# Kernel optimization log

Hardware: AMD Instinct MI355X
Metric: run time of the kernel (lower is better)

Reference implementation:

```python
import jax, jax.numpy as jnp
import numpy as np

N, E, IN, HID, H, G = 50000, 400000, 128, 16, 11, 64
HC = HID * H  # 176
OUT, NC = 32, 10
EPS = 1e-5


def setup_inputs() -> dict:
    key = jax.random.key(0)
    ks = jax.random.split(key, 20)
    def n(i, shape, s=0.05):
        return jax.random.normal(ks[i], shape, jnp.float32) * s
    inp = {}
    inp["x"] = jax.random.normal(ks[0], (N, IN), jnp.float32)
    inp["edge_index"] = jax.random.randint(ks[1], (2, E), 0, N, dtype=jnp.int32)
    inp["batch"] = jnp.sort(jax.random.randint(ks[2], (N,), 0, G, dtype=jnp.int32))
    inp["W_pre"] = n(3, (IN, HC)); inp["b_pre"] = jnp.zeros((HC,), jnp.float32)
    # GraphNorm params for gn_pre, gn1..gn4 stacked: [5, HC]
    inp["gn_w"] = jnp.ones((5, HC), jnp.float32)
    inp["gn_b"] = jnp.zeros((5, HC), jnp.float32)
    inp["gn_ms"] = jnp.ones((5, HC), jnp.float32)  # mean_scale
    # conv1..conv4 (concat=True) stacked params
    inp["conv_Wl"] = n(4, (4, HC, HC)); inp["conv_Wr"] = n(5, (4, HC, HC))
    inp["conv_att"] = n(6, (4, H, HID))
    inp["conv_b"] = jnp.zeros((4, HC), jnp.float32)
    inp["conv_Wres"] = n(7, (4, HC, HC))
    # conv5 (concat=False -> out dim HID)
    inp["c5_Wl"] = n(8, (HC, HC)); inp["c5_Wr"] = n(9, (HC, HC))
    inp["c5_att"] = n(10, (H, HID))
    inp["c5_b"] = jnp.zeros((HID,), jnp.float32)
    inp["c5_Wres"] = n(11, (HC, HID))
    inp["W_o1"] = n(12, (HID, HID)); inp["b_o1"] = jnp.zeros((HID,), jnp.float32)
    inp["W_o2"] = n(13, (HID, OUT)); inp["b_o2"] = jnp.zeros((OUT,), jnp.float32)
    inp["W_cls"] = n(14, (OUT, NC)); inp["b_cls"] = jnp.zeros((NC,), jnp.float32)
    return inp


def graph_norm(x, w, b, ms, batch, cnt):
    # PyG GraphNorm: out = w * (x - ms*mean) / sqrt(var + eps) + b, stats per graph
    mean = jax.ops.segment_sum(x, batch, G) / cnt  # [G, F]
    xc = x - mean[batch] * ms
    var = jax.ops.segment_sum(xc * xc, batch, G) / cnt
    std = jnp.sqrt(var + EPS)
    return w * xc / std[batch] + b


def gatv2_conv(x, Wl, Wr, att, bias, Wres, src, dst, concat):
    # src/dst already include self-loops (PyG add_self_loops=True)
    xl = (x @ Wl).reshape(N, H, -1)  # source transform [N,H,C]
    xr = (x @ Wr).reshape(N, H, -1)  # target transform [N,H,C]
    e = jax.nn.leaky_relu(xl[src] + xr[dst], 0.2)          # [E',H,C]
    alpha = jnp.einsum('ehc,hc->eh', e, att)               # [E',H]
    amax = jax.ops.segment_max(alpha, dst, N)
    amax = jnp.where(jnp.isfinite(amax), amax, 0.0)
    ex = jnp.exp(alpha - amax[dst])
    den = jax.ops.segment_sum(ex, dst, N)
    a = ex / (den[dst] + 1e-16)
    out = jax.ops.segment_sum(xl[src] * a[..., None], dst, N)  # [N,H,C]
    out = out.reshape(N, -1) if concat else out.mean(axis=1)
    return out + x @ Wres + bias


def reference(x, edge_index, batch, W_pre, b_pre, gn_w, gn_b, gn_ms,
              conv_Wl, conv_Wr, conv_att, conv_b, conv_Wres,
              c5_Wl, c5_Wr, c5_att, c5_b, c5_Wres,
              W_o1, b_o1, W_o2, b_o2, W_cls, b_cls):
    loops = jnp.arange(N, dtype=edge_index.dtype)
    src = jnp.concatenate([edge_index[0], loops])
    dst = jnp.concatenate([edge_index[1], loops])
    cnt = jax.ops.segment_sum(jnp.ones((N, 1), jnp.float32), batch, G)
    cnt = jnp.maximum(cnt, 1.0)  # guard empty graphs

    h = x @ W_pre + b_pre
    h = graph_norm(h, gn_w[0], gn_b[0], gn_ms[0], batch, cnt)
    h = jax.nn.relu(h)
    for i in range(4):
        h = gatv2_conv(h, conv_Wl[i], conv_Wr[i], conv_att[i], conv_b[i],
                       conv_Wres[i], src, dst, concat=True)
        h = graph_norm(h, gn_w[i + 1], gn_b[i + 1], gn_ms[i + 1], batch, cnt)
        h = jax.nn.relu(h)
    h = gatv2_conv(h, c5_Wl, c5_Wr, c5_att, c5_b, c5_Wres, src, dst, concat=False)
    h = jax.nn.relu(h)
    h = jax.nn.relu(h @ W_o1 + b_o1)
    h = jax.nn.relu(h @ W_o2 + b_o2)
    return h @ W_cls + b_cls
```

## Files before the change

kernel.cpp:

```cpp
#include <hip/hip_runtime.h>
#include <math.h>

#define N_NODES 50000
#define N_EDGES 400000
#define IN_F 128
#define HC 176
#define NGRAPH 64
#define NBLK_ATTN 12500
#define NCHUNK 16

typedef _Float16 half8 __attribute__((ext_vector_type(8)));
typedef _Float16 half4 __attribute__((ext_vector_type(4)));
typedef float floatx4 __attribute__((ext_vector_type(4)));

__device__ inline float4 h4f(const _Float16* p) {
  half4 h = *(const half4*)p;
  return make_float4((float)h[0], (float)h[1], (float)h[2], (float)h[3]);
}

#define PREH 45056
#define MATH 67584
#define TOT_PAIRS 495616
#define KCBYTES 22528
#define GX8 49

__global__ void prep_kernel(const float* __restrict__ Wpre,
                            const float* __restrict__ cWl, const float* __restrict__ cWr,
                            const float* __restrict__ cWres,
                            const float* __restrict__ c5Wl, const float* __restrict__ c5Wr,
                            _Float16* __restrict__ wp) {
  int gid = blockIdx.x * 256 + threadIdx.x;
  if (gid >= TOT_PAIRS) return;
  int mat, idx;
  if (gid < 22528) { mat = 0; idx = gid; }
  else { int g = gid - 22528; mat = 1 + g / 33792; idx = g % 33792; }
  int kc = idx / 5632;
  int rem = idx - kc * 5632;
  int ct = rem / 512;
  int li = rem - ct * 512;
  int lane = li >> 3, j = li & 7;
  int k = kc * 32 + ((lane >> 4) << 3) + j;
  int col = ct * 16 + (lane & 15);
  const float* src; int Ksrc; size_t base;
  if (mat == 0) { src = Wpre; Ksrc = 128; base = 0; }
  else if (mat <= 12) {
    int lm = mat - 1; int layer = lm / 3; int sub = lm - layer * 3;
    const float* s = (sub == 0) ? cWl : (sub == 1) ? cWr : cWres;
    src = s + (size_t)layer * HC * HC; Ksrc = HC;
    base = PREH + (size_t)lm * MATH;
  } else {
    src = (mat == 13) ? c5Wl : c5Wr; Ksrc = HC;
    base = PREH + (size_t)12 * MATH + (size_t)(mat - 13) * MATH;
  }
  float v = (k < Ksrc) ? src[(size_t)k * HC + col] : 0.0f;
  _Float16 h = (_Float16)v;
  _Float16 l = (_Float16)(v - (float)h);
  size_t o = base + (size_t)(kc * 11 + ct) * 1024 + li;
  wp[o] = h;
  wp[o + 512] = l;
}

template <int MINW, bool DOSTATS, bool AHALF>
__global__ __launch_bounds__(256, MINW) void gemm_mfma_t(
    const float* __restrict__ A, int M, int K, int nkc, int nmat,
    const _Float16* __restrict__ Wp, int matStride,
    const float* __restrict__ scsh, const int* __restrict__ batch,
    const float* __restrict__ bias0, const float* __restrict__ bias1,
    const float* __restrict__ bias2,
    float* __restrict__ out0, float* __restrict__ out1, float* __restrict__ out2,
    float* __restrict__ parts, float* __restrict__ partq, float* __restrict__ stats,
    int halfMask) {
  __shared__ __align__(16) char smem[2 * KCBYTES];
  const int b = blockIdx.x;
  const int grp = b >> 3, sub = b & 7;
  const int mat = grp % nmat;
  const int tile = ((grp / nmat) << 3) | sub;
  if (tile * 128 >= M) return;
  const _Float16* W = Wp + (size_t)mat * matStride;
  float* outp = (mat == 0) ? out0 : (mat == 1) ? out1 : out2;
  const float* bias = (mat == 0) ? bias0 : (mat == 1) ? bias1 : bias2;
  const bool hOut = (halfMask >> mat) & 1;
  const int tid = threadIdx.x;
  const int lane = tid & 63;
  const int wv = tid >> 6;
  const int m16 = lane & 15, quad = lane >> 4;
  const int kb = quad << 3;
  const int rowBase = tile * 128 + wv * 32;
  const int rA0 = min(rowBase + m16, M - 1);
  const int rA1 = min(rowBase + 16 + m16, M - 1);
  const float* ap0 = A + (size_t)rA0 * K + kb;
  const float* ap1 = A + (size_t)rA1 * K + kb;
  const _Float16* hp0 = (const _Float16*)A + (size_t)rA0 * K + kb;
  const _Float16* hp1 = (const _Float16*)A + (size_t)rA1 * K + kb;
  const float* sc0 = nullptr; const float* sh0 = nullptr;
  const float* sc1 = nullptr; const float* sh1 = nullptr;
  if (scsh) {
    int g0 = batch[rA0], g1 = batch[rA1];
    sc0 = scsh + (size_t)g0 * HC + kb;
    sh0 = scsh + (size_t)(NGRAPH + g0) * HC + kb;
    sc1 = scsh + (size_t)g1 * HC + kb;
    sh1 = scsh + (size_t)(NGRAPH + g1) * HC + kb;
  }

  auto stage = [&](int kc, int buf) {
    const char* src = (const char*)W + (size_t)kc * KCBYTES;
    char* dst = smem + buf * KCBYTES;
#pragma unroll
    for (int i = 0; i < 6; i++) {
      int idx = wv * 6 + i;
      if (idx < 22) {
        __builtin_amdgcn_global_load_lds(
            (const __attribute__((address_space(1))) unsigned int*)(src + idx * 1024 + lane * 16),
            (__attribute__((address_space(3))) unsigned int*)(dst + idx * 1024),
            16, 0, 0);
      }
    }
  };

  floatx4 acc0[11], acc1[11];
#pragma unroll
  for (int ct = 0; ct < 11; ct++)
#pragma unroll
    for (int r = 0; r < 4; r++) { acc0[ct][r] = 0.0f; acc1[ct][r] = 0.0f; }

  stage(0, 0);

  for (int kc = 0; kc < nkc; kc++) {
    const int buf = kc & 1;
    __syncthreads();
    if (kc + 1 < nkc) stage(kc + 1, 1 - buf);

    const int koff = kc << 5;
    float va0[8], va1[8];
    if (koff + kb + 8 <= K) {
      if (AHALF) {
        half8 u = *(const half8*)(hp0 + koff);
        half8 w = *(const half8*)(hp1 + koff);
#pragma unroll
        for (int j = 0; j < 8; j++) { va0[j] = (float)u[j]; va1[j] = (float)w[j]; }
      } else {
        float4 u0 = *(const float4*)(ap0 + koff);
        float4 u1 = *(const float4*)(ap0 + koff + 4);
        float4 w0 = *(const float4*)(ap1 + koff);
        float4 w1 = *(const float4*)(ap1 + koff + 4);
        va0[0] = u0.x; va0[1] = u0.y; va0[2] = u0.z; va0[3] = u0.w;
        va0[4] = u1.x; va0[5] = u1.y; va0[6] = u1.z; va0[7] = u1.w;
        va1[0] = w0.x; va1[1] = w0.y; va1[2] = w0.z; va1[3] = w0.w;
        va1[4] = w1.x; va1[5] = w1.y; va1[6] = w1.z; va1[7] = w1.w;
      }
      if (scsh) {
        float s0[8], h0[8], s1[8], h1[8];
        float4 t;
        t = *(const float4*)(sc0 + koff);     s0[0]=t.x; s0[1]=t.y; s0[2]=t.z; s0[3]=t.w;
        t = *(const float4*)(sc0 + koff + 4); s0[4]=t.x; s0[5]=t.y; s0[6]=t.z; s0[7]=t.w;
        t = *(const float4*)(sh0 + koff);     h0[0]=t.x; h0[1]=t.y; h0[2]=t.z; h0[3]=t.w;
        t = *(const float4*)(sh0 + koff + 4); h0[4]=t.x; h0[5]=t.y; h0[6]=t.z; h0[7]=t.w;
        t = *(const float4*)(sc1 + koff);     s1[0]=t.x; s1[1]=t.y; s1[2]=t.z; s1[3]=t.w;
        t = *(const float4*)(sc1 + koff + 4); s1[4]=t.x; s1[5]=t.y; s1[6]=t.z; s1[7]=t.w;
        t = *(const float4*)(sh1 + koff);     h1[0]=t.x; h1[1]=t.y; h1[2]=t.z; h1[3]=t.w;
        t = *(const float4*)(sh1 + koff + 4); h1[4]=t.x; h1[5]=t.y; h1[6]=t.z; h1[7]=t.w;
#pragma unroll
        for (int j = 0; j < 8; j++) {
          va0[j] = fmaxf(fmaf(va0[j], s0[j], h0[j]), 0.0f);
          va1[j] = fmaxf(fmaf(va1[j], s1[j], h1[j]), 0.0f);
        }
      }
    } else {
#pragma unroll
      for (int j = 0; j < 8; j++) { va0[j] = 0.0f; va1[j] = 0.0f; }
    }
    half8 ah0, al0, ah1, al1;
#pragma unroll
    for (int j = 0; j < 8; j++) {
      _Float16 h = (_Float16)va0[j];
      ah0[j] = h; al0[j] = (_Float16)(va0[j] - (float)h);
      _Float16 g = (_Float16)va1[j];
      ah1[j] = g; al1[j] = (_Float16)(va1[j] - (float)g);
    }
    const char* bbase = smem + buf * KCBYTES + lane * 16;
#pragma unroll
    for (int ct = 0; ct < 11; ct++) {
      half8 bh = *(const half8*)(bbase + ct * 2048);
      half8 bl = *(const half8*)(bbase + ct * 2048 + 1024);
      acc0[ct] = __builtin_amdgcn_mfma_f32_16x16x32_f16(ah0, bh, acc0[ct], 0, 0, 0);
      acc1[ct] = __builtin_amdgcn_mfma_f32_16x16x32_f16(ah1, bh, acc1[ct], 0, 0, 0);
      acc0[ct] = __builtin_amdgcn_mfma_f32_16x16x32_f16(al0, bh, acc0[ct], 0, 0, 0);
      acc1[ct] = __builtin_amdgcn_mfma_f32_16x16x32_f16(al1, bh, acc1[ct], 0, 0, 0);
      acc0[ct] = __builtin_amdgcn_mfma_f32_16x16x32_f16(ah0, bl, acc0[ct], 0, 0, 0);
      acc1[ct] = __builtin_amdgcn_mfma_f32_16x16x32_f16(ah1, bl, acc1[ct], 0, 0, 0);
    }
  }

  float bv[11];
#pragma unroll
  for (int ct = 0; ct < 11; ct++) bv[ct] = bias ? bias[ct * 16 + m16] : 0.0f;
#pragma unroll
  for (int r = 0; r < 4; r++) {
    int row0 = rowBase + (quad << 2) + r;
    if (row0 < M) {
      if (hOut) {
        _Float16* op = (_Float16*)outp + (size_t)row0 * HC + m16;
#pragma unroll
        for (int ct = 0; ct < 11; ct++) op[ct * 16] = (_Float16)(acc0[ct][r] + bv[ct]);
      } else {
        float* op = outp + (size_t)row0 * HC + m16;
#pragma unroll
        for (int ct = 0; ct < 11; ct++) op[ct * 16] = acc0[ct][r] + bv[ct];
      }
    }
    int row1 = row0 + 16;
    if (row1 < M) {
      if (hOut) {
        _Float16* op = (_Float16*)outp + (size_t)row1 * HC + m16;
#pragma unroll
        for (int ct = 0; ct < 11; ct++) op[ct * 16] = (_Float16)(acc1[ct][r] + bv[ct]);
      } else {
        float* op = outp + (size_t)row1 * HC + m16;
#pragma unroll
        for (int ct = 0; ct < 11; ct++) op[ct * 16] = acc1[ct][r] + bv[ct];
      }
    }
  }

  if (DOSTATS) {
    int gTile = batch[tile * 128];
    int lastRow = min(tile * 128 + 127, M - 1);
    bool straddle = (batch[lastRow] != gTile);
    bool validR[8]; bool otherR[8];
#pragma unroll
    for (int r = 0; r < 4; r++) {
      int row0 = rowBase + (quad << 2) + r;
      validR[r] = (row0 < M);
      otherR[r] = validR[r] && (batch[min(row0, M - 1)] != gTile);
      int row1 = row0 + 16;
      validR[4 + r] = (row1 < M);
      otherR[4 + r] = validR[4 + r] && (batch[min(row1, M - 1)] != gTile);
    }
    __syncthreads();
    float* red = (float*)smem;
#pragma unroll
    for (int ct = 0; ct < 11; ct++) {
      float sA = 0.f, qA = 0.f, sB = 0.f, qB = 0.f;
#pragma unroll
      for (int r = 0; r < 4; r++) {
        if (validR[r]) {
          float v = acc0[ct][r] + bv[ct];
          if (otherR[r]) { sB += v; qB = fmaf(v, v, qB); }
          else           { sA += v; qA = fmaf(v, v, qA); }
        }
        if (validR[4 + r]) {
          float v = acc1[ct][r] + bv[ct];
          if (otherR[4 + r]) { sB += v; qB = fmaf(v, v, qB); }
          else               { sA += v; qA = fmaf(v, v, qA); }
        }
      }
      sA += __shfl_xor(sA, 16); sA += __shfl_xor(sA, 32);
      qA += __shfl_xor(qA, 16); qA += __shfl_xor(qA, 32);
      sB += __shfl_xor(sB, 16); sB += __shfl_xor(sB, 32);
      qB += __shfl_xor(qB, 16); qB += __shfl_xor(qB, 32);
      if (quad == 0) {
        float* slot = red + (((wv * 11 + ct) * 16 + m16) << 2);
        slot[0] = sA; slot[1] = qA; slot[2] = sB; slot[3] = qB;
      }
    }
    __syncthreads();
    if (tid < HC) {
      int col = tid;
      float sA = 0.f, qA = 0.f, sB = 0.f, qB = 0.f;
#pragma unroll
      for (int w = 0; w < 4; w++) {
        float* slot = red + (((w * 11 + col / 16) * 16 + (col & 15)) << 2);
        sA += slot[0]; qA += slot[1]; sB += slot[2]; qB += slot[3];
      }
      parts[(size_t)tile * HC + col] = sA;
      partq[(size_t)tile * HC + col] = qA;
      if (straddle) {
        int g2 = batch[lastRow];
        atomicAdd(&stats[g2 * HC + col], sB);
        atomicAdd(&stats[(NGRAPH + g2) * HC + col], qB);
      }
    }
  }
}

__global__ __launch_bounds__(256) void part_reduce_kernel(
    const float* __restrict__ parts, const float* __restrict__ partq,
    const int* __restrict__ gstart, float* __restrict__ stats, int rpb) {
  int idx = blockIdx.x * 256 + threadIdx.x;
  if (idx >= NGRAPH * NCHUNK * HC) return;
  int f = idx % HC;
  int gc = idx / HC;
  int g = gc / NCHUNK, c = gc % NCHUNK;
  int s0 = gstart[g], s1 = gstart[g + 1];
  int b0 = (s0 + rpb - 1) / rpb, b1 = (s1 + rpb - 1) / rpb;
  int len = b1 - b0;
  if (len <= 0) return;
  int per = (len + NCHUNK - 1) / NCHUNK;
  int cb0 = b0 + c * per;
  int cb1 = min(cb0 + per, b1);
  if (cb0 >= cb1) return;
  float s = 0.f, ss = 0.f;
  for (int b = cb0; b < cb1; b++) {
    s += parts[(size_t)b * HC + f];
    ss += partq[(size_t)b * HC + f];
  }
  atomicAdd(&stats[g * HC + f], s);
  atomicAdd(&stats[(NGRAPH + g) * HC + f], ss);
}

__global__ void gn_finalize_kernel(const float* __restrict__ stats, const int* __restrict__ cntInt,
                                   const float* __restrict__ gnw, const float* __restrict__ gnb,
                                   const float* __restrict__ gnms, int row,
                                   float* __restrict__ scsh) {
  int i = blockIdx.x * 256 + threadIdx.x;
  if (i >= NGRAPH * HC) return;
  int g = i / HC, f = i - g * HC;
  float c = fmaxf((float)cntInt[g], 1.0f);
  float m = stats[i] / c;
  float sq = stats[NGRAPH * HC + i] / c;
  float ms = gnms[row * HC + f];
  float var = sq - m * m * ms * (2.0f - ms);
  float w = gnw[row * HC + f], b = gnb[row * HC + f];
  float scale = w / sqrtf(var + 1e-5f);
  float shift = b - scale * ms * m;
  scsh[i] = scale;
  scsh[NGRAPH * HC + i] = shift;
}

__global__ void cnt_bsearch_kernel(const int* __restrict__ batch, int* __restrict__ cntInt,
                                   int* __restrict__ gstart) {
  int g = threadIdx.x;
  if (g >= NGRAPH) return;
  auto lb = [&](int v) {
    int lo = 0, hi = N_NODES;
    while (lo < hi) {
      int mid = (lo + hi) >> 1;
      if (batch[mid] < v) lo = mid + 1; else hi = mid;
    }
    return lo;
  };
  int a = lb(g), b = lb(g + 1);
  cntInt[g] = b - a;
  gstart[g] = a;
  if (g == NGRAPH - 1) gstart[NGRAPH] = N_NODES;
}

__global__ void deg_hist_kernel(const int* __restrict__ dstE, int* __restrict__ deg) {
  int e = blockIdx.x * 256 + threadIdx.x;
  if (e < N_EDGES) atomicAdd(&deg[dstE[e]], 1);
}

__global__ void scan1_kernel(const int* __restrict__ deg, int* __restrict__ bsum) {
  __shared__ int sd[256];
  int i = blockIdx.x * 256 + threadIdx.x;
  sd[threadIdx.x] = (i < N_NODES) ? deg[i] : 0;
  __syncthreads();
  for (int s = 128; s > 0; s >>= 1) {
    if (threadIdx.x < s) sd[threadIdx.x] += sd[threadIdx.x + s];
    __syncthreads();
  }
  if (threadIdx.x == 0) bsum[blockIdx.x] = sd[0];
}

__global__ void scan2_kernel(int* __restrict__ bsum, int nb) {
  __shared__ int sd[256];
  int t = threadIdx.x;
  int v0 = (t < nb) ? bsum[t] : 0;
  sd[t] = v0;
  __syncthreads();
  for (int s = 1; s < 256; s <<= 1) {
    int v = (t >= s) ? sd[t - s] : 0;
    __syncthreads();
    sd[t] += v;
    __syncthreads();
  }
  if (t < nb) bsum[t] = sd[t] - v0;
}

__global__ void scan3_kernel(const int* __restrict__ deg, const int* __restrict__ bsum,
                             int* __restrict__ rowptr) {
  __shared__ int sd[256];
  int i = blockIdx.x * 256 + threadIdx.x;
  int t = threadIdx.x;
  int d = (i < N_NODES) ? deg[i] : 0;
  sd[t] = d;
  __syncthreads();
  for (int s = 1; s < 256; s <<= 1) {
    int v = (t >= s) ? sd[t - s] : 0;
    __syncthreads();
    sd[t] += v;
    __syncthreads();
  }
  if (i < N_NODES) rowptr[i] = bsum[blockIdx.x] + sd[t] - d;
  if (i == 0) rowptr[N_NODES] = N_EDGES;
}

__global__ void scatter_kernel(const int* __restrict__ srcE, const int* __restrict__ dstE,
                               const int* __restrict__ rowptr, int* __restrict__ fill,
                               int* __restrict__ colA) {
  int e = blockIdx.x * 256 + threadIdx.x;
  if (e < N_EDGES) {
    int d = dstE[e];
    int pos = rowptr[d] + atomicAdd(&fill[d], 1);
    colA[pos] = srcE[e];
  }
}

#define AEDGE(V, D, ACC)                                                      \
  do {                                                                        \
    float e0 = (V).x + xrv.x; e0 = fmaxf(e0, 0.2f * e0);                      \
    float e1 = (V).y + xrv.y; e1 = fmaxf(e1, 0.2f * e1);                      \
    float e2 = (V).z + xrv.z; e2 = fmaxf(e2, 0.2f * e2);                      \
    float e3 = (V).w + xrv.w; e3 = fmaxf(e3, 0.2f * e3);                      \
    float p = fmaf(e3, av.w, fmaf(e2, av.z, fmaf(e1, av.y, e0 * av.x)));      \
    p += __shfl_xor(p, 1);                                                    \
    p += __shfl_xor(p, 2);                                                    \
    float pp = __expf(p);                                                     \
    (D) += pp;                                                                \
    (ACC).x = fmaf(pp, (V).x, (ACC).x);                                       \
    (ACC).y = fmaf(pp, (V).y, (ACC).y);                                       \
    (ACC).z = fmaf(pp, (V).z, (ACC).z);                                       \
    (ACC).w = fmaf(pp, (V).w, (ACC).w);                                       \
  } while (0)

__global__ __launch_bounds__(256) void attn_concat_kernel(
    const _Float16* __restrict__ xl, const _Float16* __restrict__ xr,
    const float* __restrict__ att, const int* __restrict__ rowptr,
    const int* __restrict__ colA, _Float16* __restrict__ out,
    const int* __restrict__ batch, float* __restrict__ stats,
    float* __restrict__ parts, float* __restrict__ partq) {
  __shared__ float sv[4 * HC];
  int t = threadIdx.x;
  int node = blockIdx.x * 4 + (t >> 6);
  int lane = t & 63;
  if (lane < 44) {
    const float4 av = *(const float4*)(att + lane * 4);
    size_t base = (size_t)node * HC + lane * 4;
    const float4 xrv = h4f(xr + base);
    int start = rowptr[node], end = rowptr[node + 1];
    float d = 0.0f, dB = 0.0f;
    float4 acc = make_float4(0.f, 0.f, 0.f, 0.f);
    float4 accB = make_float4(0.f, 0.f, 0.f, 0.f);
    float4 p1, p2;
    if (start < end)     p1 = h4f(xl + (size_t)colA[start] * HC + lane * 4);
    if (start + 1 < end) p2 = h4f(xl + (size_t)colA[start + 1] * HC + lane * 4);
    {
      float4 svv = h4f(xl + base);
      AEDGE(svv, d, acc);
    }
    int j = start;
    for (; j + 3 < end; j += 2) {
      float4 n1 = h4f(xl + (size_t)colA[j + 2] * HC + lane * 4);
      float4 n2 = h4f(xl + (size_t)colA[j + 3] * HC + lane * 4);
      AEDGE(p1, d, acc);
      AEDGE(p2, dB, accB);
      p1 = n1; p2 = n2;
    }
    if (j < end)     AEDGE(p1, d, acc);
    if (j + 1 < end) AEDGE(p2, dB, accB);
    if (j + 2 < end) {
      float4 n1 = h4f(xl + (size_t)colA[j + 2] * HC + lane * 4);
      AEDGE(n1, d, acc);
    }
    d += dB;
    acc.x += accB.x; acc.y += accB.y; acc.z += accB.z; acc.w += accB.w;
    float rd = 1.0f / (d + 1e-16f);
    half4 rv = *(const half4*)(out + base);
    float4 o;
    o.x = fmaf(acc.x, rd, (float)rv[0]);
    o.y = fmaf(acc.y, rd, (float)rv[1]);
    o.z = fmaf(acc.z, rd, (float)rv[2]);
    o.w = fmaf(acc.w, rd, (float)rv[3]);
    half4 st;
    st[0] = (_Float16)o.x; st[1] = (_Float16)o.y;
    st[2] = (_Float16)o.z; st[3] = (_Float16)o.w;
    *(half4*)(out + base) = st;
    *(float4*)(&sv[(t >> 6) * HC + lane * 4]) = o;
  }
  __syncthreads();
  if (t < HC) {
    int b = blockIdx.x;
    int g0 = batch[b * 4];
    float s = 0.0f, ss = 0.0f;
#pragma unroll
    for (int w = 0; w < 4; w++) {
      int g = batch[b * 4 + w];
      float v = sv[w * HC + t];
      if (g == g0) {
        s += v;
        ss = fmaf(v, v, ss);
      } else {
        atomicAdd(&stats[g * HC + t], v);
        atomicAdd(&stats[(NGRAPH + g) * HC + t], v * v);
      }
    }
    parts[(size_t)b * HC + t] = s;
    partq[(size_t)b * HC + t] = ss;
  }
}

__global__ __launch_bounds__(256) void attn_mean_kernel(
    const _Float16* __restrict__ xl, const _Float16* __restrict__ xr,
    const float* __restrict__ att, const int* __restrict__ rowptr,
    const int* __restrict__ colA, const float* __restrict__ res16,
    float* __restrict__ out16) {
  int t = threadIdx.x;
  int node = blockIdx.x * 4 + (t >> 6);
  int lane = t & 63;
  if (node >= N_NODES) return;
  int L = (lane < 44) ? lane : 0;
  const float4 av = *(const float4*)(att + L * 4);
  size_t base = (size_t)node * HC + L * 4;
  const float4 xrv = h4f(xr + base);
  int start = rowptr[node], end = rowptr[node + 1];
  float d = 0.0f, dB = 0.0f;
  float4 acc = make_float4(0.f, 0.f, 0.f, 0.f);
  float4 accB = make_float4(0.f, 0.f, 0.f, 0.f);
  float4 p1, p2;
  if (start < end)     p1 = h4f(xl + (size_t)colA[start] * HC + L * 4);
  if (start + 1 < end) p2 = h4f(xl + (size_t)colA[start + 1] * HC + L * 4);
  {
    float4 svv = h4f(xl + base);
    AEDGE(svv, d, acc);
  }
  int j = start;
  for (; j + 3 < end; j += 2) {
    float4 n1 = h4f(xl + (size_t)colA[j + 2] * HC + L * 4);
    float4 n2 = h4f(xl + (size_t)colA[j + 3] * HC + L * 4);
    AEDGE(p1, d, acc);
    AEDGE(p2, dB, accB);
    p1 = n1; p2 = n2;
  }
  if (j < end)     AEDGE(p1, d, acc);
  if (j + 1 < end) AEDGE(p2, dB, accB);
  if (j + 2 < end) {
    float4 n1 = h4f(xl + (size_t)colA[j + 2] * HC + L * 4);
    AEDGE(n1, d, acc);
  }
  d += dB;
  acc.x += accB.x; acc.y += accB.y; acc.z += accB.z; acc.w += accB.w;
  float rd = 1.0f / (d + 1e-16f);
  float4 o;
  o.x = (lane < 44) ? acc.x * rd : 0.0f;
  o.y = (lane < 44) ? acc.y * rd : 0.0f;
  o.z = (lane < 44) ? acc.z * rd : 0.0f;
  o.w = (lane < 44) ? acc.w * rd : 0.0f;
#pragma unroll
  for (int w = 4; w <= 32; w <<= 1) {
    o.x += __shfl_xor(o.x, w);
    o.y += __shfl_xor(o.y, w);
    o.z += __shfl_xor(o.z, w);
    o.w += __shfl_xor(o.w, w);
  }
  if (lane < 4) {
    const float* rp = res16 + (size_t)node * 16 + lane * 4;
    float4 r = *(const float4*)rp;
    float4 ov;
    ov.x = fmaxf(fmaf(o.x, 1.0f / 11.0f, r.x), 0.0f);
    ov.y = fmaxf(fmaf(o.y, 1.0f / 11.0f, r.y), 0.0f);
    ov.z = fmaxf(fmaf(o.z, 1.0f / 11.0f, r.z), 0.0f);
    ov.w = fmaxf(fmaf(o.w, 1.0f / 11.0f, r.w), 0.0f);
    *(float4*)(out16 + (size_t)node * 16 + lane * 4) = ov;
  }
}

__global__ __launch_bounds__(256) void res16_kernel(const _Float16* __restrict__ h,
                                                    const float* __restrict__ scsh,
                                                    const int* __restrict__ batch,
                                                    const float* __restrict__ Wres,
                                                    const float* __restrict__ b16,
                                                    float* __restrict__ res16) {
  __shared__ float Ws[176 * 16];
  __shared__ float hs[16 * 176];
  int t = threadIdx.x;
  for (int i = t; i < 176 * 16; i += 256) Ws[i] = Wres[i];
  int n0 = blockIdx.x * 16;
  for (int i = t; i < 16 * 176; i += 256) {
    int row = i / 176, k = i - row * 176;
    int g = batch[n0 + row];
    float v = (float)h[(size_t)n0 * HC + i];
    hs[i] = fmaxf(fmaf(v, scsh[g * HC + k], scsh[(NGRAPH + g) * HC + k]), 0.0f);
  }
  __syncthreads();
  int tx = t & 15, ty = t >> 4;
  float acc = b16[tx];
  for (int k = 0; k < HC; k++) acc = fmaf(hs[ty * HC + k], Ws[k * 16 + tx], acc);
  res16[(size_t)(n0 + ty) * 16 + tx] = acc;
}

__global__ __launch_bounds__(256) void head_kernel(
    const float* __restrict__ in16, const float* __restrict__ Wo1,
    const float* __restrict__ bo1, const float* __restrict__ Wo2,
    const float* __restrict__ bo2, const float* __restrict__ Wc,
    const float* __restrict__ bc, float* __restrict__ outp) {
  __shared__ float w1[256], w2[512], wcS[320], b1[16], b2[32], bcS[10];
  int t = threadIdx.x;
  for (int i = t; i < 256; i += 256) w1[i] = Wo1[i];
  for (int i = t; i < 512; i += 256) w2[i] = Wo2[i];
  for (int i = t; i < 320; i += 256) wcS[i] = Wc[i];
  if (t < 16) b1[t] = bo1[t];
  if (t < 32) b2[t] = bo2[t];
  if (t < 10) bcS[t] = bc[t];
  __syncthreads();
  int n = blockIdx.x * 256 + t;
  if (n >= N_NODES) return;
  float x[16];
#pragma unroll
  for (int i = 0; i < 16; i++) x[i] = in16[(size_t)n * 16 + i];
  float o1[16];
#pragma unroll
  for (int j = 0; j < 16; j++) {
    float a = b1[j];
#pragma unroll
    for (int k = 0; k < 16; k++) a = fmaf(x[k], w1[k * 16 + j], a);
    o1[j] = fmaxf(a, 0.0f);
  }
  float o2[32];
#pragma unroll
  for (int j = 0; j < 32; j++) {
    float a = b2[j];
#pragma unroll
    for (int k = 0; k < 16; k++) a = fmaf(o1[k], w2[k * 32 + j], a);
    o2[j] = fmaxf(a, 0.0f);
  }
#pragma unroll
  for (int j = 0; j < 10; j++) {
    float a = bcS[j];
#pragma unroll
    for (int k = 0; k < 32; k++) a = fmaf(o2[k], wcS[k * 10 + j], a);
    outp[(size_t)n * 10 + j] = a;
  }
}

extern "C" void kernel_launch(void* const* d_in, const int* in_sizes, int n_in,
                              void* d_out, int out_size, void* d_ws, size_t ws_size,
                              hipStream_t stream) {
  (void)in_sizes; (void)n_in; (void)out_size; (void)ws_size;
  const float* x     = (const float*)d_in[0];
  const int*   ei    = (const int*)d_in[1];
  const int*   srcE  = ei;
  const int*   dstE  = ei + N_EDGES;
  const int*   batch = (const int*)d_in[2];
  const float* W_pre = (const float*)d_in[3];
  const float* b_pre = (const float*)d_in[4];
  const float* gn_w  = (const float*)d_in[5];
  const float* gn_b  = (const float*)d_in[6];
  const float* gn_ms = (const float*)d_in[7];
  const float* cWl   = (const float*)d_in[8];
  const float* cWr   = (const float*)d_in[9];
  const float* cAtt  = (const float*)d_in[10];
  const float* cB    = (const float*)d_in[11];
  const float* cWres = (const float*)d_in[12];
  const float* c5Wl  = (const float*)d_in[13];
  const float* c5Wr  = (const float*)d_in[14];
  const float* c5Att = (const float*)d_in[15];
  const float* c5b   = (const float*)d_in[16];
  const float* c5Wres= (const float*)d_in[17];
  const float* Wo1   = (const float*)d_in[18];
  const float* bo1   = (const float*)d_in[19];
  const float* Wo2   = (const float*)d_in[20];
  const float* bo2   = (const float*)d_in[21];
  const float* Wc    = (const float*)d_in[22];
  const float* bc    = (const float*)d_in[23];

  const size_t FB = (size_t)N_NODES * HC;
  const size_t STB = (size_t)2 * NGRAPH * HC;
  const size_t PB = (size_t)NBLK_ATTN * HC;
  float* ws    = (float*)d_ws;
  float* buf0  = ws;
  float* buf1  = ws + FB;
  float* buf2  = ws + 2 * FB;
  float* buf3  = ws + 3 * FB;
  float* res16 = ws + 4 * FB;
  float* out16 = res16 + (size_t)N_NODES * 16;
  float* stats = out16 + (size_t)N_NODES * 16;
  int* deg     = (int*)(stats + 5 * STB);
  int* fill    = deg + N_NODES;
  float* scsh  = (float*)(fill + N_NODES);
  float* parts = scsh + STB;
  float* partq = parts + PB;
  _Float16* wph = (_Float16*)(partq + PB);
  int* ibase   = (int*)((char*)wph + (size_t)991232 * 2);
  int* cntInt  = ibase;
  int* gstart  = ibase + 64;
  int* rowptr  = gstart + 65;
  int* colA    = rowptr + N_NODES + 1;
  int* bsum    = colA + N_EDGES;

  const int NB = (N_NODES + 255) / 256;

  hipMemsetAsync(stats, 0, sizeof(float) * 5 * STB + sizeof(int) * 2 * N_NODES, stream);

  prep_kernel<<<(TOT_PAIRS + 255) / 256, 256, 0, stream>>>(W_pre, cWl, cWr, cWres, c5Wl, c5Wr, wph);
  cnt_bsearch_kernel<<<1, 64, 0, stream>>>(batch, cntInt, gstart);
  deg_hist_kernel<<<(N_EDGES + 255) / 256, 256, 0, stream>>>(dstE, deg);
  scan1_kernel<<<NB, 256, 0, stream>>>(deg, bsum);
  scan2_kernel<<<1, 256, 0, stream>>>(bsum, NB);
  scan3_kernel<<<NB, 256, 0, stream>>>(deg, bsum, rowptr);
  scatter_kernel<<<(N_EDGES + 255) / 256, 256, 0, stream>>>(srcE, dstE, rowptr, fill, colA);

  const int PRB = (NGRAPH * NCHUNK * HC + 255) / 256;

  gemm_mfma_t<2, true, false><<<GX8 * 1 * 8, 256, 0, stream>>>(
      x, N_NODES, IN_F, 4, 1, wph, 0, nullptr, batch,
      b_pre, nullptr, nullptr, buf0, nullptr, nullptr,
      parts, partq, stats, 1);
  part_reduce_kernel<<<PRB, 256, 0, stream>>>(parts, partq, gstart, stats, 128);
  gn_finalize_kernel<<<(NGRAPH * HC + 255) / 256, 256, 0, stream>>>(stats, cntInt, gn_w, gn_b, gn_ms, 0, scsh);

  float* h = buf0;
  float* o = buf3;
  for (int i = 0; i < 4; i++) {
    const _Float16* Wcat_i = wph + PREH + (size_t)(3 * i) * MATH;
    gemm_mfma_t<3, false, true><<<GX8 * 3 * 8, 256, 0, stream>>>(
        h, N_NODES, HC, 6, 3, Wcat_i, MATH, scsh, batch,
        nullptr, nullptr, cB + i * HC, buf1, buf2, o,
        nullptr, nullptr, nullptr, 7);
    float* st = stats + (size_t)(i + 1) * STB;
    attn_concat_kernel<<<NBLK_ATTN, 256, 0, stream>>>((const _Float16*)buf1, (const _Float16*)buf2,
                                                      cAtt + i * HC,
                                                      rowptr, colA, (_Float16*)o, batch, st,
                                                      parts, partq);
    part_reduce_kernel<<<PRB, 256, 0, stream>>>(parts, partq, gstart, st, 4);
    gn_finalize_kernel<<<(NGRAPH * HC + 255) / 256, 256, 0, stream>>>(st, cntInt, gn_w, gn_b, gn_ms, i + 1, scsh);
    float* tmp = h; h = o; o = tmp;
  }

  const _Float16* Wc5 = wph + PREH + (size_t)12 * MATH;
  gemm_mfma_t<3, false, true><<<GX8 * 2 * 8, 256, 0, stream>>>(
      h, N_NODES, HC, 6, 2, Wc5, MATH, scsh, batch,
      nullptr, nullptr, nullptr, buf1, buf2, nullptr,
      nullptr, nullptr, nullptr, 3);
  res16_kernel<<<N_NODES / 16, 256, 0, stream>>>((const _Float16*)h, scsh, batch, c5Wres, c5b, res16);
  attn_mean_kernel<<<(N_NODES + 3) / 4, 256, 0, stream>>>((const _Float16*)buf1, (const _Float16*)buf2,
                                                          c5Att, rowptr, colA, res16, out16);

  head_kernel<<<NB, 256, 0, stream>>>(out16, Wo1, bo1, Wo2, bo2, Wc, bc, (float*)d_out);
}
```

Measured before the change: 705.4 us.

## Split each node's edge aggregation across two wavefronts and combine via LDS

Each node's neighbor loop in both attention kernels is now split between two wavefronts that take interleaved edge pairs. Their partial softmax numerators and denominators are combined through shared memory. This doubles the block count and halves the per-wave serial gather chain, aiming at more memory-level parallelism for the latency-bound gather. The parts/partq partial buffers are moved into the unused upper halves of buf1/buf2, and the partial reduce stride is updated. The cost is an extra LDS reduction and barrier per block, plus idle lanes (44 of 64 are active) across more waves.

After: 796.7 us. 1.13x slower.

```diff
diff --git a/kernel.cpp b/kernel.cpp
--- a/kernel.cpp
+++ b/kernel.cpp
@@ -6,7 +6,7 @@
 #define IN_F 128
 #define HC 176
 #define NGRAPH 64
-#define NBLK_ATTN 12500
+#define NBLK_ATTN 25000
 #define NCHUNK 16
 
 typedef _Float16 half8 __attribute__((ext_vector_type(8)));
@@ -423,47 +423,65 @@
     (ACC).w = fmaf(pp, (V).w, (ACC).w);                                       \
   } while (0)
 
+#define ATTN_HALF_BODY(XLL)                                                   \
+  int start = rowptr[node], end = rowptr[node + 1];                           \
+  float dB = 0.0f;                                                            \
+  float4 accB = make_float4(0.f, 0.f, 0.f, 0.f);                              \
+  float4 p1, p2;                                                              \
+  int j = start + wvp;                                                        \
+  if (j < end)     p1 = h4f(xl + (size_t)colA[j] * HC + (XLL));               \
+  if (j + 2 < end) p2 = h4f(xl + (size_t)colA[j + 2] * HC + (XLL));           \
+  if (wvp == 0) {                                                             \
+    float4 svv = h4f(xl + base);                                              \
+    AEDGE(svv, d, acc);                                                       \
+  }                                                                           \
+  for (; j + 6 < end; j += 4) {                                               \
+    float4 n1 = h4f(xl + (size_t)colA[j + 4] * HC + (XLL));                   \
+    float4 n2 = h4f(xl + (size_t)colA[j + 6] * HC + (XLL));                   \
+    AEDGE(p1, d, acc);                                                        \
+    AEDGE(p2, dB, accB);                                                      \
+    p1 = n1; p2 = n2;                                                         \
+  }                                                                           \
+  if (j < end)     AEDGE(p1, d, acc);                                         \
+  if (j + 2 < end) AEDGE(p2, dB, accB);                                       \
+  if (j + 4 < end) {                                                          \
+    float4 n1 = h4f(xl + (size_t)colA[j + 4] * HC + (XLL));                   \
+    AEDGE(n1, d, acc);                                                        \
+  }                                                                           \
+  d += dB;                                                                    \
+  acc.x += accB.x; acc.y += accB.y; acc.z += accB.z; acc.w += accB.w;
+
 __global__ __launch_bounds__(256) void attn_concat_kernel(
     const _Float16* __restrict__ xl, const _Float16* __restrict__ xr,
     const float* __restrict__ att, const int* __restrict__ rowptr,
     const int* __restrict__ colA, _Float16* __restrict__ out,
     const int* __restrict__ batch, float* __restrict__ stats,
     float* __restrict__ parts, float* __restrict__ partq) {
-  __shared__ float sv[4 * HC];
+  __shared__ float sv[2 * HC];
+  __shared__ float red[2][44][5];
   int t = threadIdx.x;
-  int node = blockIdx.x * 4 + (t >> 6);
+  int pair = t >> 7;
+  int wvp = (t >> 6) & 1;
   int lane = t & 63;
+  int node = blockIdx.x * 2 + pair;
+  float d = 0.0f;
+  float4 acc = make_float4(0.f, 0.f, 0.f, 0.f);
+  size_t base = (size_t)node * HC + lane * 4;
   if (lane < 44) {
     const float4 av = *(const float4*)(att + lane * 4);
-    size_t base = (size_t)node * HC + lane * 4;
     const float4 xrv = h4f(xr + base);
-    int start = rowptr[node], end = rowptr[node + 1];
-    float d = 0.0f, dB = 0.0f;
-    float4 acc = make_float4(0.f, 0.f, 0.f, 0.f);
-    float4 accB = make_float4(0.f, 0.f, 0.f, 0.f);
-    float4 p1, p2;
-    if (start < end)     p1 = h4f(xl + (size_t)colA[start] * HC + lane * 4);
-    if (start + 1 < end) p2 = h4f(xl + (size_t)colA[start + 1] * HC + lane * 4);
-    {
-      float4 svv = h4f(xl + base);
-      AEDGE(svv, d, acc);
-    }
-    int j = start;
-    for (; j + 3 < end; j += 2) {
-      float4 n1 = h4f(xl + (size_t)colA[j + 2] * HC + lane * 4);
-      float4 n2 = h4f(xl + (size_t)colA[j + 3] * HC + lane * 4);
-      AEDGE(p1, d, acc);
-      AEDGE(p2, dB, accB);
-      p1 = n1; p2 = n2;
-    }
-    if (j < end)     AEDGE(p1, d, acc);
-    if (j + 1 < end) AEDGE(p2, dB, accB);
-    if (j + 2 < end) {
-      float4 n1 = h4f(xl + (size_t)colA[j + 2] * HC + lane * 4);
-      AEDGE(n1, d, acc);
-    }
-    d += dB;
-    acc.x += accB.x; acc.y += accB.y; acc.z += accB.z; acc.w += accB.w;
+    ATTN_HALF_BODY(lane * 4)
+    if (wvp == 1) {
+      red[pair][lane][0] = d;
+      red[pair][lane][1] = acc.x; red[pair][lane][2] = acc.y;
+      red[pair][lane][3] = acc.z; red[pair][lane][4] = acc.w;
+    }
+  }
+  __syncthreads();
+  if (wvp == 0 && lane < 44) {
+    d += red[pair][lane][0];
+    acc.x += red[pair][lane][1]; acc.y += red[pair][lane][2];
+    acc.z += red[pair][lane][3]; acc.w += red[pair][lane][4];
     float rd = 1.0f / (d + 1e-16f);
     half4 rv = *(const half4*)(out + base);
     float4 o;
@@ -475,16 +493,16 @@
     st[0] = (_Float16)o.x; st[1] = (_Float16)o.y;
     st[2] = (_Float16)o.z; st[3] = (_Float16)o.w;
     *(half4*)(out + base) = st;
-    *(float4*)(&sv[(t >> 6) * HC + lane * 4]) = o;
+    *(float4*)(&sv[pair * HC + lane * 4]) = o;
   }
   __syncthreads();
   if (t < HC) {
     int b = blockIdx.x;
-    int g0 = batch[b * 4];
+    int g0 = batch[b * 2];
     float s = 0.0f, ss = 0.0f;
 #pragma unroll
-    for (int w = 0; w < 4; w++) {
-      int g = batch[b * 4 + w];
+    for (int w = 0; w < 2; w++) {
+      int g = batch[b * 2 + w];
       float v = sv[w * HC + t];
       if (g == g0) {
         s += v;
@@ -504,63 +522,56 @@
     const float* __restrict__ att, const int* __restrict__ rowptr,
     const int* __restrict__ colA, const float* __restrict__ res16,
     float* __restrict__ out16) {
+  __shared__ float red[2][44][5];
   int t = threadIdx.x;
-  int node = blockIdx.x * 4 + (t >> 6);
+  int pair = t >> 7;
+  int wvp = (t >> 6) & 1;
   int lane = t & 63;
-  if (node >= N_NODES) return;
+  int node = blockIdx.x * 2 + pair;
   int L = (lane < 44) ? lane : 0;
   const float4 av = *(const float4*)(att + L * 4);
   size_t base = (size_t)node * HC + L * 4;
   const float4 xrv = h4f(xr + base);
-  int start = rowptr[node], end = rowptr[node + 1];
-  float d = 0.0f, dB = 0.0f;
+  float d = 0.0f;
   float4 acc = make_float4(0.f, 0.f, 0.f, 0.f);
-  float4 accB = make_float4(0.f, 0.f, 0.f, 0.f);
-  float4 p1, p2;
-  if (start < end)     p1 = h4f(xl + (size_t)colA[start] * HC + L * 4);
-  if (start + 1 < end) p2 = h4f(xl + (size_t)colA[start + 1] * HC + L * 4);
   {
-    float4 svv = h4f(xl + base);
-    AEDGE(svv, d, acc);
-  }
-  int j = start;
-  for (; j + 3 < end; j += 2) {
-    float4 n1 = h4f(xl + (size_t)colA[j + 2] * HC + L * 4);
-    float4 n2 = h4f(xl + (size_t)colA[j + 3] * HC + L * 4);
-    AEDGE(p1, d, acc);
-    AEDGE(p2, dB, accB);
-    p1 = n1; p2 = n2;
-  }
-  if (j < end)     AEDGE(p1, d, acc);
-  if (j + 1 < end) AEDGE(p2, dB, accB);
-  if (j + 2 < end) {
-    float4 n1 = h4f(xl + (size_t)colA[j + 2] * HC + L * 4);
-    AEDGE(n1, d, acc);
-  }
-  d += dB;
-  acc.x += accB.x; acc.y += accB.y; acc.z += accB.z; acc.w += accB.w;
-  float rd = 1.0f / (d + 1e-16f);
-  float4 o;
-  o.x = (lane < 44) ? acc.x * rd : 0.0f;
-  o.y = (lane < 44) ? acc.y * rd : 0.0f;
-  o.z = (lane < 44) ? acc.z * rd : 0.0f;
-  o.w = (lane < 44) ? acc.w * rd : 0.0f;
-#pragma unroll
-  for (int w = 4; w <= 32; w <<= 1) {
-    o.x += __shfl_xor(o.x, w);
-    o.y += __shfl_xor(o.y, w);
-    o.z += __shfl_xor(o.z, w);
-    o.w += __shfl_xor(o.w, w);
-  }
-  if (lane < 4) {
-    const float* rp = res16 + (size_t)node * 16 + lane * 4;
-    float4 r = *(const float4*)rp;
-    float4 ov;
-    ov.x = fmaxf(fmaf(o.x, 1.0f / 11.0f, r.x), 0.0f);
-    ov.y = fmaxf(fmaf(o.y, 1.0f / 11.0f, r.y), 0.0f);
-    ov.z = fmaxf(fmaf(o.z, 1.0f / 11.0f, r.z), 0.0f);
-    ov.w = fmaxf(fmaf(o.w, 1.0f / 11.0f, r.w), 0.0f);
-    *(float4*)(out16 + (size_t)node * 16 + lane * 4) = ov;
+    ATTN_HALF_BODY(L * 4)
+  }
+  if (wvp == 1 && lane < 44) {
+    red[pair][lane][0] = d;
+    red[pair][lane][1] = acc.x; red[pair][lane][2] = acc.y;
+    red[pair][lane][3] = acc.z; red[pair][lane][4] = acc.w;
+  }
+  __syncthreads();
+  if (wvp == 0) {
+    if (lane < 44) {
+      d += red[pair][lane][0];
+      acc.x += red[pair][lane][1]; acc.y += red[pair][lane][2];
+      acc.z += red[pair][lane][3]; acc.w += red[pair][lane][4];
+    }
+    float rd = 1.0f / (d + 1e-16f);
+    float4 o;
+    o.x = (lane < 44) ? acc.x * rd : 0.0f;
+    o.y = (lane < 44) ? acc.y * rd : 0.0f;
+    o.z = (lane < 44) ? acc.z * rd : 0.0f;
+    o.w = (lane < 44) ? acc.w * rd : 0.0f;
+#pragma unroll
+    for (int w = 4; w <= 32; w <<= 1) {
+      o.x += __shfl_xor(o.x, w);
+      o.y += __shfl_xor(o.y, w);
+      o.z += __shfl_xor(o.z, w);
+      o.w += __shfl_xor(o.w, w);
+    }
+    if (lane < 4) {
+      const float* rp = res16 + (size_t)node * 16 + lane * 4;
+      float4 r = *(const float4*)rp;
+      float4 ov;
+      ov.x = fmaxf(fmaf(o.x, 1.0f / 11.0f, r.x), 0.0f);
+      ov.y = fmaxf(fmaf(o.y, 1.0f / 11.0f, r.y), 0.0f);
+      ov.z = fmaxf(fmaf(o.z, 1.0f / 11.0f, r.z), 0.0f);
+      ov.w = fmaxf(fmaf(o.w, 1.0f / 11.0f, r.w), 0.0f);
+      *(float4*)(out16 + (size_t)node * 16 + lane * 4) = ov;
+    }
   }
 }
 
@@ -665,7 +676,7 @@
 
   const size_t FB = (size_t)N_NODES * HC;
   const size_t STB = (size_t)2 * NGRAPH * HC;
-  const size_t PB = (size_t)NBLK_ATTN * HC;
+  const size_t PBOLD = (size_t)12500 * HC;
   float* ws    = (float*)d_ws;
   float* buf0  = ws;
   float* buf1  = ws + FB;
@@ -677,15 +688,16 @@
   int* deg     = (int*)(stats + 5 * STB);
   int* fill    = deg + N_NODES;
   float* scsh  = (float*)(fill + N_NODES);
-  float* parts = scsh + STB;
-  float* partq = parts + PB;
-  _Float16* wph = (_Float16*)(partq + PB);
+  float* partsOld = scsh + STB;
+  _Float16* wph = (_Float16*)(partsOld + 2 * PBOLD);
   int* ibase   = (int*)((char*)wph + (size_t)991232 * 2);
   int* cntInt  = ibase;
   int* gstart  = ibase + 64;
   int* rowptr  = gstart + 65;
   int* colA    = rowptr + N_NODES + 1;
   int* bsum    = colA + N_EDGES;
+  float* parts = buf1 + FB / 2;
+  float* partq = buf2 + FB / 2;
 
   const int NB = (N_NODES + 255) / 256;
 
@@ -721,7 +733,7 @@
                                                       cAtt + i * HC,
                                                       rowptr, colA, (_Float16*)o, batch, st,
                                                       parts, partq);
-    part_reduce_kernel<<<PRB, 256, 0, stream>>>(parts, partq, gstart, st, 4);
+    part_reduce_kernel<<<PRB, 256, 0, stream>>>(parts, partq, gstart, st, 2);
     gn_finalize_kernel<<<(NGRAPH * HC + 255) / 256, 256, 0, stream>>>(st, cntInt, gn_w, gn_b, gn_ms, i + 1, scsh);
     float* tmp = h; h = o; o = tmp;
   }
@@ -732,8 +744,8 @@
       nullptr, nullptr, nullptr, buf1, buf2, nullptr,
       nullptr, nullptr, nullptr, 3);
   res16_kernel<<<N_NODES / 16, 256, 0, stream>>>((const _Float16*)h, scsh, batch, c5Wres, c5b, res16);
-  attn_mean_kernel<<<(N_NODES + 3) / 4, 256, 0, stream>>>((const _Float16*)buf1, (const _Float16*)buf2,
-                                                          c5Att, rowptr, colA, res16, out16);
+  attn_mean_kernel<<<NBLK_ATTN, 256, 0, stream>>>((const _Float16*)buf1, (const _Float16*)buf2,
+                                                  c5Att, rowptr, colA, res16, out16);
 
   head_kernel<<<NB, 256, 0, stream>>>(out16, Wo1, bo1, Wo2, bo2, Wc, bc, (float*)d_out);
 }
```

## Replace partial-sum buffers and reduce kernel with chunked atomic GraphNorm stats

Applied to the files above, without the earlier changes.

Removes the per-block partial sum buffers and the separate part_reduce_kernel launch. Producers now atomically add into per-graph, per-chunk stat slots (16 chunks per graph, to spread contention), and gn_finalize sums the chunks. Separately, the gather row index in the attention loop goes through readfirstlane so address math can be scalar, and the loop is factored into a shared macro. In exchange the stats buffer grows and memset gets larger, and float atomics make the summation order nondeterministic.

Result: no change. 692.6 us (-1.8%).

```diff
diff --git a/kernel.cpp b/kernel.cpp
--- a/kernel.cpp
+++ b/kernel.cpp
@@ -8,6 +8,7 @@
 #define NGRAPH 64
 #define NBLK_ATTN 12500
 #define NCHUNK 16
+#define SQOFF (NGRAPH * NCHUNK * HC)
 
 typedef _Float16 half8 __attribute__((ext_vector_type(8)));
 typedef _Float16 half4 __attribute__((ext_vector_type(4)));
@@ -16,6 +17,10 @@
 __device__ inline float4 h4f(const _Float16* p) {
   half4 h = *(const half4*)p;
   return make_float4((float)h[0], (float)h[1], (float)h[2], (float)h[3]);
+}
+
+__device__ inline const _Float16* urow(const _Float16* p, int c) {
+  return p + (size_t)(unsigned)__builtin_amdgcn_readfirstlane(c) * HC;
 }
 
 #define PREH 45056
@@ -68,8 +73,7 @@
     const float* __restrict__ bias0, const float* __restrict__ bias1,
     const float* __restrict__ bias2,
     float* __restrict__ out0, float* __restrict__ out1, float* __restrict__ out2,
-    float* __restrict__ parts, float* __restrict__ partq, float* __restrict__ stats,
-    int halfMask) {
+    float* __restrict__ stats, int halfMask) {
   __shared__ __align__(16) char smem[2 * KCBYTES];
   const int b = blockIdx.x;
   const int grp = b >> 3, sub = b & 7;
@@ -272,40 +276,16 @@
         float* slot = red + (((w * 11 + col / 16) * 16 + (col & 15)) << 2);
         sA += slot[0]; qA += slot[1]; sB += slot[2]; qB += slot[3];
       }
-      parts[(size_t)tile * HC + col] = sA;
-      partq[(size_t)tile * HC + col] = qA;
+      int chunk = tile & (NCHUNK - 1);
+      atomicAdd(&stats[(gTile * NCHUNK + chunk) * HC + col], sA);
+      atomicAdd(&stats[SQOFF + (gTile * NCHUNK + chunk) * HC + col], qA);
       if (straddle) {
         int g2 = batch[lastRow];
-        atomicAdd(&stats[g2 * HC + col], sB);
-        atomicAdd(&stats[(NGRAPH + g2) * HC + col], qB);
-      }
-    }
-  }
-}
-
-__global__ __launch_bounds__(256) void part_reduce_kernel(
-    const float* __restrict__ parts, const float* __restrict__ partq,
-    const int* __restrict__ gstart, float* __restrict__ stats, int rpb) {
-  int idx = blockIdx.x * 256 + threadIdx.x;
-  if (idx >= NGRAPH * NCHUNK * HC) return;
-  int f = idx % HC;
-  int gc = idx / HC;
-  int g = gc / NCHUNK, c = gc % NCHUNK;
-  int s0 = gstart[g], s1 = gstart[g + 1];
-  int b0 = (s0 + rpb - 1) / rpb, b1 = (s1 + rpb - 1) / rpb;
-  int len = b1 - b0;
-  if (len <= 0) return;
-  int per = (len + NCHUNK - 1) / NCHUNK;
-  int cb0 = b0 + c * per;
-  int cb1 = min(cb0 + per, b1);
-  if (cb0 >= cb1) return;
-  float s = 0.f, ss = 0.f;
-  for (int b = cb0; b < cb1; b++) {
-    s += parts[(size_t)b * HC + f];
-    ss += partq[(size_t)b * HC + f];
-  }
-  atomicAdd(&stats[g * HC + f], s);
-  atomicAdd(&stats[(NGRAPH + g) * HC + f], ss);
+        atomicAdd(&stats[(g2 * NCHUNK + chunk) * HC + col], sB);
+        atomicAdd(&stats[SQOFF + (g2 * NCHUNK + chunk) * HC + col], qB);
+      }
+    }
+  }
 }
 
 __global__ void gn_finalize_kernel(const float* __restrict__ stats, const int* __restrict__ cntInt,
@@ -315,11 +295,17 @@
   int i = blockIdx.x * 256 + threadIdx.x;
   if (i >= NGRAPH * HC) return;
   int g = i / HC, f = i - g * HC;
-  float c = fmaxf((float)cntInt[g], 1.0f);
-  float m = stats[i] / c;
-  float sq = stats[NGRAPH * HC + i] / c;
+  float sm = 0.f, sq = 0.f;
+#pragma unroll
+  for (int c = 0; c < NCHUNK; c++) {
+    sm += stats[(g * NCHUNK + c) * HC + f];
+    sq += stats[SQOFF + (g * NCHUNK + c) * HC + f];
+  }
+  float cnt = fmaxf((float)cntInt[g], 1.0f);
+  float m = sm / cnt;
+  float msq = sq / cnt;
   float ms = gnms[row * HC + f];
-  float var = sq - m * m * ms * (2.0f - ms);
+  float var = msq - m * m * ms * (2.0f - ms);
   float w = gnw[row * HC + f], b = gnb[row * HC + f];
   float scale = w / sqrtf(var + 1e-5f);
   float shift = b - scale * ms * m;
@@ -423,12 +409,40 @@
     (ACC).w = fmaf(pp, (V).w, (ACC).w);                                       \
   } while (0)
 
+#define ATTN_BODY(XLL)                                                        \
+  int start = rowptr[node], end = rowptr[node + 1];                           \
+  float d = 0.0f, dB = 0.0f;                                                  \
+  float4 acc = make_float4(0.f, 0.f, 0.f, 0.f);                               \
+  float4 accB = make_float4(0.f, 0.f, 0.f, 0.f);                              \
+  float4 p1, p2;                                                              \
+  if (start < end)     p1 = h4f(urow(xl, colA[start]) + (XLL));               \
+  if (start + 1 < end) p2 = h4f(urow(xl, colA[start + 1]) + (XLL));           \
+  {                                                                           \
+    float4 svv = h4f(xl + base);                               \
+    AEDGE(svv, d, acc);                                                       \
+  }                                                                           \
+  int j = start;                                                              \
+  for (; j + 3 < end; j += 2) {                                               \
+    float4 n1 = h4f(urow(xl, colA[j + 2]) + (XLL));                           \
+    float4 n2 = h4f(urow(xl, colA[j + 3]) + (XLL));                           \
+    AEDGE(p1, d, acc);                                                        \
+    AEDGE(p2, dB, accB);                                                      \
+    p1 = n1; p2 = n2;                                                         \
+  }                                                                           \
+  if (j < end)     AEDGE(p1, d, acc);                                         \
+  if (j + 1 < end) AEDGE(p2, dB, accB);                                       \
+  if (j + 2 < end) {                                                          \
+    float4 n1 = h4f(urow(xl, colA[j + 2]) + (XLL));                           \
+    AEDGE(n1, d, acc);                                                        \
+  }                                                                           \
+  d += dB;                                                                    \
+  acc.x += accB.x; acc.y += accB.y; acc.z += accB.z; acc.w += accB.w;
+
 __global__ __launch_bounds__(256) void attn_concat_kernel(
     const _Float16* __restrict__ xl, const _Float16* __restrict__ xr,
     const float* __restrict__ att, const int* __restrict__ rowptr,
     const int* __restrict__ colA, _Float16* __restrict__ out,
-    const int* __restrict__ batch, float* __restrict__ stats,
-    float* __restrict__ parts, float* __restrict__ partq) {
+    const int* __restrict__ batch, float* __restrict__ stats) {
   __shared__ float sv[4 * HC];
   int t = threadIdx.x;
   int node = blockIdx.x * 4 + (t >> 6);
@@ -437,35 +451,9 @@
     const float4 av = *(const float4*)(att + lane * 4);
     size_t base = (size_t)node * HC + lane * 4;
     const float4 xrv = h4f(xr + base);
-    int start = rowptr[node], end = rowptr[node + 1];
-    float d = 0.0f, dB = 0.0f;
-    float4 acc = make_float4(0.f, 0.f, 0.f, 0.f);
-    float4 accB = make_float4(0.f, 0.f, 0.f, 0.f);
-    float4 p1, p2;
-    if (start < end)     p1 = h4f(xl + (size_t)colA[start] * HC + lane * 4);
-    if (start + 1 < end) p2 = h4f(xl + (size_t)colA[start + 1] * HC + lane * 4);
-    {
-      float4 svv = h4f(xl + base);
-      AEDGE(svv, d, acc);
-    }
-    int j = start;
-    for (; j + 3 < end; j += 2) {
-      float4 n1 = h4f(xl + (size_t)colA[j + 2] * HC + lane * 4);
-      float4 n2 = h4f(xl + (size_t)colA[j + 3] * HC + lane * 4);
-      AEDGE(p1, d, acc);
-      AEDGE(p2, dB, accB);
-      p1 = n1; p2 = n2;
-    }
-    if (j < end)     AEDGE(p1, d, acc);
-    if (j + 1 < end) AEDGE(p2, dB, accB);
-    if (j + 2 < end) {
-      float4 n1 = h4f(xl + (size_t)colA[j + 2] * HC + lane * 4);
-      AEDGE(n1, d, acc);
-    }
-    d += dB;
-    acc.x += accB.x; acc.y += accB.y; acc.z += accB.z; acc.w += accB.w;
+    half4 rv = *(const half4*)(out + base);
+    ATTN_BODY(lane * 4)
     float rd = 1.0f / (d + 1e-16f);
-    half4 rv = *(const half4*)(out + base);
     float4 o;
     o.x = fmaf(acc.x, rd, (float)rv[0]);
     o.y = fmaf(acc.y, rd, (float)rv[1]);
@@ -480,8 +468,11 @@
   __syncthreads();
   if (t < HC) {
     int b = blockIdx.x;
+    int chunk = b & (NCHUNK - 1);
     int g0 = batch[b * 4];
     float s = 0.0f, ss = 0.0f;
+    float sB = 0.0f, ssB = 0.0f;
+    int gB = -1;
 #pragma unroll
     for (int w = 0; w < 4; w++) {
       int g = batch[b * 4 + w];
@@ -490,12 +481,15 @@
         s += v;
         ss = fmaf(v, v, ss);
       } else {
-        atomicAdd(&stats[g * HC + t], v);
-        atomicAdd(&stats[(NGRAPH + g) * HC + t], v * v);
-      }
-    }
-    parts[(size_t)b * HC + t] = s;
-    partq[(size_t)b * HC + t] = ss;
+        gB = g; sB += v; ssB = fmaf(v, v, ssB);
+      }
+    }
+    atomicAdd(&stats[(g0 * NCHUNK + chunk) * HC + t], s);
+    atomicAdd(&stats[SQOFF + (g0 * NCHUNK + chunk) * HC + t], ss);
+    if (gB >= 0) {
+      atomicAdd(&stats[(gB * NCHUNK + chunk) * HC + t], sB);
+      atomicAdd(&stats[SQOFF + (gB * NCHUNK + chunk) * HC + t], ssB);
+    }
   }
 }
 
@@ -512,33 +506,7 @@
   const float4 av = *(const float4*)(att + L * 4);
   size_t base = (size_t)node * HC + L * 4;
   const float4 xrv = h4f(xr + base);
-  int start = rowptr[node], end = rowptr[node + 1];
-  float d = 0.0f, dB = 0.0f;
-  float4 acc = make_float4(0.f, 0.f, 0.f, 0.f);
-  float4 accB = make_float4(0.f, 0.f, 0.f, 0.f);
-  float4 p1, p2;
-  if (start < end)     p1 = h4f(xl + (size_t)colA[start] * HC + L * 4);
-  if (start + 1 < end) p2 = h4f(xl + (size_t)colA[start + 1] * HC + L * 4);
-  {
-    float4 svv = h4f(xl + base);
-    AEDGE(svv, d, acc);
-  }
-  int j = start;
-  for (; j + 3 < end; j += 2) {
-    float4 n1 = h4f(xl + (size_t)colA[j + 2] * HC + L * 4);
-    float4 n2 = h4f(xl + (size_t)colA[j + 3] * HC + L * 4);
-    AEDGE(p1, d, acc);
-    AEDGE(p2, dB, accB);
-    p1 = n1; p2 = n2;
-  }
-  if (j < end)     AEDGE(p1, d, acc);
-  if (j + 1 < end) AEDGE(p2, dB, accB);
-  if (j + 2 < end) {
-    float4 n1 = h4f(xl + (size_t)colA[j + 2] * HC + L * 4);
-    AEDGE(n1, d, acc);
-  }
-  d += dB;
-  acc.x += accB.x; acc.y += accB.y; acc.z += accB.z; acc.w += accB.w;
+  ATTN_BODY(L * 4)
   float rd = 1.0f / (d + 1e-16f);
   float4 o;
   o.x = (lane < 44) ? acc.x * rd : 0.0f;
@@ -664,8 +632,7 @@
   const float* bc    = (const float*)d_in[23];
 
   const size_t FB = (size_t)N_NODES * HC;
-  const size_t STB = (size_t)2 * NGRAPH * HC;
-  const size_t PB = (size_t)NBLK_ATTN * HC;
+  const size_t STB2 = (size_t)2 * NGRAPH * NCHUNK * HC;
   float* ws    = (float*)d_ws;
   float* buf0  = ws;
   float* buf1  = ws + FB;
@@ -673,13 +640,11 @@
   float* buf3  = ws + 3 * FB;
   float* res16 = ws + 4 * FB;
   float* out16 = res16 + (size_t)N_NODES * 16;
-  float* stats = out16 + (size_t)N_NODES * 16;
-  int* deg     = (int*)(stats + 5 * STB);
+  float* stats2 = out16 + (size_t)N_NODES * 16;
+  int* deg     = (int*)(stats2 + 5 * STB2);
   int* fill    = deg + N_NODES;
   float* scsh  = (float*)(fill + N_NODES);
-  float* parts = scsh + STB;
-  float* partq = parts + PB;
-  _Float16* wph = (_Float16*)(partq + PB);
+  _Float16* wph = (_Float16*)(scsh + (size_t)2 * NGRAPH * HC);
   int* ibase   = (int*)((char*)wph + (size_t)991232 * 2);
   int* cntInt  = ibase;
   int* gstart  = ibase + 64;
@@ -689,7 +654,7 @@
 
   const int NB = (N_NODES + 255) / 256;
 
-  hipMemsetAsync(stats, 0, sizeof(float) * 5 * STB + sizeof(int) * 2 * N_NODES, stream);
+  hipMemsetAsync(stats2, 0, sizeof(float) * 5 * STB2 + sizeof(int) * 2 * N_NODES, stream);
 
   prep_kernel<<<(TOT_PAIRS + 255) / 256, 256, 0, stream>>>(W_pre, cWl, cWr, cWres, c5Wl, c5Wr, wph);
   cnt_bsearch_kernel<<<1, 64, 0, stream>>>(batch, cntInt, gstart);
@@ -699,14 +664,11 @@
   scan3_kernel<<<NB, 256, 0, stream>>>(deg, bsum, rowptr);
   scatter_kernel<<<(N_EDGES + 255) / 256, 256, 0, stream>>>(srcE, dstE, rowptr, fill, colA);
 
-  const int PRB = (NGRAPH * NCHUNK * HC + 255) / 256;
-
   gemm_mfma_t<2, true, false><<<GX8 * 1 * 8, 256, 0, stream>>>(
       x, N_NODES, IN_F, 4, 1, wph, 0, nullptr, batch,
       b_pre, nullptr, nullptr, buf0, nullptr, nullptr,
-      parts, partq, stats, 1);
-  part_reduce_kernel<<<PRB, 256, 0, stream>>>(parts, partq, gstart, stats, 128);
-  gn_finalize_kernel<<<(NGRAPH * HC + 255) / 256, 256, 0, stream>>>(stats, cntInt, gn_w, gn_b, gn_ms, 0, scsh);
+      stats2, 1);
+  gn_finalize_kernel<<<(NGRAPH * HC + 255) / 256, 256, 0, stream>>>(stats2, cntInt, gn_w, gn_b, gn_ms, 0, scsh);
 
   float* h = buf0;
   float* o = buf3;
@@ -715,13 +677,11 @@
     gemm_mfma_t<3, false, true><<<GX8 * 3 * 8, 256, 0, stream>>>(
         h, N_NODES, HC, 6, 3, Wcat_i, MATH, scsh, batch,
         nullptr, nullptr, cB + i * HC, buf1, buf2, o,
-        nullptr, nullptr, nullptr, 7);
-    float* st = stats + (size_t)(i + 1) * STB;
+        nullptr, 7);
+    float* st = stats2 + (size_t)(i + 1) * STB2;
     attn_concat_kernel<<<NBLK_ATTN, 256, 0, stream>>>((const _Float16*)buf1, (const _Float16*)buf2,
                                                       cAtt + i * HC,
-                                                      rowptr, colA, (_Float16*)o, batch, st,
-                                                      parts, partq);
-    part_reduce_kernel<<<PRB, 256, 0, stream>>>(parts, partq, gstart, st, 4);
+                                                      rowptr, colA, (_Float16*)o, batch, st);
     gn_finalize_kernel<<<(NGRAPH * HC + 255) / 256, 256, 0, stream>>>(st, cntInt, gn_w, gn_b, gn_ms, i + 1, scsh);
     float* tmp = h; h = o; o = tmp;
   }
@@ -730,7 +690,7 @@
   gemm_mfma_t<3, false, true><<<GX8 * 2 * 8, 256, 0, stream>>>(
       h, N_NODES, HC, 6, 2, Wc5, MATH, scsh, batch,
       nullptr, nullptr, nullptr, buf1, buf2, nullptr,
-      nullptr, nullptr, nullptr, 3);
+      nullptr, 3);
   res16_kernel<<<N_NODES / 16, 256, 0, stream>>>((const _Float16*)h, scsh, batch, c5Wres, c5b, res16);
   attn_mean_kernel<<<(N_NODES + 3) / 4, 256, 0, stream>>>((const _Float16*)buf1, (const _Float16*)buf2,
                                                           c5Att, rowptr, colA, res16, out16);
```
